# Optimization experiments

Measured on AMD Instinct MI355X. Metric: run time of the kernel, lower is better.

The kernel has to match this reference:

```python
import jax, jax.numpy as jnp
import numpy as np

LOG_STD_MAX = 2.0
LOG_STD_MIN = -5.0
LN_EPS = 1e-5


def layer_norm(x, scale, bias):
    mu = jnp.mean(x, axis=-1, keepdims=True)
    var = jnp.var(x, axis=-1, keepdims=True)
    return (x - mu) * jax.lax.rsqrt(var + LN_EPS) * scale + bias


def setup_inputs() -> dict:
    key = jax.random.key(0)
    B, OBS, ACT, H, M, K = 4096, 256, 32, 512, 16, 4
    ks = jax.random.split(key, 8)
    def w(k, shape, fan_in):
        return (jax.random.normal(k, shape, jnp.float32) / np.sqrt(fan_in)).astype(jnp.float32)
    return {
        "x": jax.random.normal(ks[0], (B, OBS), jnp.float32),
        "gate_W": w(ks[1], (OBS, M), OBS),
        "gate_b": jnp.zeros((M,), jnp.float32),
        "fc1_W": w(ks[2], (OBS, H * M), OBS),
        "fc1_b": jnp.zeros((H * M,), jnp.float32),
        "norm1_scale": jnp.ones((H * M,), jnp.float32),
        "norm1_bias": jnp.zeros((H * M,), jnp.float32),
        "fc2_W": w(ks[3], (H * M, H * M), H * M),
        "fc2_b": jnp.zeros((H * M,), jnp.float32),
        "norm2_scale": jnp.ones((H * M,), jnp.float32),
        "norm2_bias": jnp.zeros((H * M,), jnp.float32),
        "mean_W": w(ks[4], (H, ACT), H),
        "mean_b": jnp.zeros((ACT,), jnp.float32),
        "logstd_W": w(ks[5], (H, ACT), H),
        "logstd_b": jnp.zeros((ACT,), jnp.float32),
        "topk": K,
    }


def reference(x, gate_W, gate_b, fc1_W, fc1_b, norm1_scale, norm1_bias,
              fc2_W, fc2_b, norm2_scale, norm2_bias,
              mean_W, mean_b, logstd_W, logstd_b, topk):
    B = x.shape[0]
    M = gate_W.shape[1]
    # gating: softmax -> topk -> renormalize -> scatter into full [B, M] scores
    gate_scores = jax.nn.softmax(x @ gate_W + gate_b, axis=-1)  # [B, M]
    topk_vals, topk_idx = jax.lax.top_k(gate_scores, topk)       # [B, K]
    topk_vals = topk_vals / jnp.sum(topk_vals, axis=-1, keepdims=True)
    scores = jnp.zeros_like(gate_scores).at[jnp.arange(B)[:, None], topk_idx].set(topk_vals)
    # trunk: Linear -> LayerNorm -> ReLU, twice
    h = jax.nn.relu(layer_norm(x @ fc1_W + fc1_b, norm1_scale, norm1_bias))
    h = jax.nn.relu(layer_norm(h @ fc2_W + fc2_b, norm2_scale, norm2_bias))
    # reshape [B, H*M] -> [B, H, M] (expert m = strided slice), weighted MEAN over experts
    h = h.reshape(B, -1, M)                                      # [B, H, M]
    mixed = jnp.einsum('bhm,bm->bh', h, scores) / M              # mean, not sum
    mean = mixed @ mean_W + mean_b
    log_std = jnp.tanh(mixed @ logstd_W + logstd_b)
    log_std = LOG_STD_MIN + 0.5 * (LOG_STD_MAX - LOG_STD_MIN) * (log_std + 1.0)
    return mean, log_std
```

## Files before the change

kernel.cpp:

```cpp
#include <hip/hip_runtime.h>
#include <hip/hip_bf16.h>

typedef unsigned int u32;
typedef unsigned short u16;
typedef __bf16 bf16x8 __attribute__((ext_vector_type(8)));
typedef float f32x4 __attribute__((ext_vector_type(4)));

__device__ __forceinline__ u16 f2b(float f) {
    __bf16 b = (__bf16)f;
    return __builtin_bit_cast(u16, b);
}
__device__ __forceinline__ float b2f(u16 v) {
    u32 x = ((u32)v) << 16;
    return __builtin_bit_cast(float, x);
}

__device__ __forceinline__ void gld_lds16(const void* g, void* l) {
    __builtin_amdgcn_global_load_lds(
        (const __attribute__((address_space(1))) u32*)(size_t)g,
        (__attribute__((address_space(3))) u32*)(u32)(size_t)l,
        16, 0, 0);
}

#define BARRIER __builtin_amdgcn_s_barrier()
#define LGKM0 asm volatile("s_waitcnt lgkmcnt(0)" ::: "memory")
#define VMC4 asm volatile("s_waitcnt vmcnt(4)" ::: "memory")
#define VMC6 asm volatile("s_waitcnt vmcnt(6)" ::: "memory")
#define VMC0 asm volatile("s_waitcnt vmcnt(0)" ::: "memory")
#define MFMA16(d, a, b) d = __builtin_amdgcn_mfma_f32_16x16x32_bf16(a, b, d, 0, 0, 0)

__global__ __launch_bounds__(256) void castgate_kernel(
    const float* __restrict__ x, const float* __restrict__ gW,
    const float* __restrict__ gb, const int* __restrict__ topk,
    u16* __restrict__ XB, float* __restrict__ scores)
{
    const int t = threadIdx.x;
    {
        int i = blockIdx.x * 256 + t;
        float4 f = reinterpret_cast<const float4*>(x)[i];
        u32 lo = (u32)f2b(f.x) | ((u32)f2b(f.y) << 16);
        u32 hi = (u32)f2b(f.z) | ((u32)f2b(f.w) << 16);
        uint2 o; o.x = lo; o.y = hi;
        reinterpret_cast<uint2*>(XB)[i] = o;
    }
    const int row = blockIdx.x * 4 + (t >> 6);
    const int l = t & 63;
    const int m = l & 15;
    const int q = l >> 4;
    const int Kk = *topk;
    const float* xr = x + (long)row * 256;
    float p = 0.f;
    #pragma unroll
    for (int k4 = 0; k4 < 16; ++k4) {
        f32x4 xv = *reinterpret_cast<const f32x4*>(xr + q * 64 + k4 * 4);
        const int kb = q * 64 + k4 * 4;
        p += xv[0] * gW[(kb + 0) * 16 + m] + xv[1] * gW[(kb + 1) * 16 + m]
           + xv[2] * gW[(kb + 2) * 16 + m] + xv[3] * gW[(kb + 3) * 16 + m];
    }
    p += __shfl_xor(p, 16);
    p += __shfl_xor(p, 32);
    float logit = p + gb[m];
    float mx = logit;
    #pragma unroll
    for (int d = 1; d < 16; d <<= 1) mx = fmaxf(mx, __shfl_xor(mx, d));
    int rank = 0;
    #pragma unroll
    for (int j = 0; j < 16; ++j) {
        float vj = __shfl(logit, (l & 48) | j);
        rank += (vj > logit) || (vj == logit && j < m);
    }
    bool sel = rank < Kk;
    float e = sel ? expf(logit - mx) : 0.f;
    float ssum = e;
    #pragma unroll
    for (int d = 1; d < 16; d <<= 1) ssum += __shfl_xor(ssum, d);
    if (q == 0) scores[row * 16 + m] = e / ssum;
}

__global__ __launch_bounds__(256) void transpose_both_kernel(
    const float* __restrict__ w2, u16* __restrict__ W2T,
    const float* __restrict__ w1, u16* __restrict__ W1T)
{
    __shared__ float tile[64][65];
    const int t = threadIdx.x;
    const int byy = blockIdx.y;
    const float* in;
    u16* outp;
    int R, r0;
    if (byy < 128) { in = w2; outp = W2T; R = 8192; r0 = byy * 64; }
    else           { in = w1; outp = W1T; R = 256;  r0 = (byy - 128) * 64; }
    const int C = 8192;
    const int c0 = blockIdx.x * 64;
    #pragma unroll
    for (int i = 0; i < 4; ++i) {
        int idx = t + i * 256;
        int r = idx >> 4;
        int c = (idx & 15) * 4;
        float4 f = *reinterpret_cast<const float4*>(&in[(long)(r0 + r) * C + c0 + c]);
        tile[r][c] = f.x; tile[r][c + 1] = f.y; tile[r][c + 2] = f.z; tile[r][c + 3] = f.w;
    }
    __syncthreads();
    #pragma unroll
    for (int i = 0; i < 8; ++i) {
        int idx = t + i * 256;
        int rr = idx >> 5;
        int cc = idx & 31;
        u32 p = (u32)f2b(tile[cc * 2 + 0][rr]) | ((u32)f2b(tile[cc * 2 + 1][rr]) << 16);
        *reinterpret_cast<u32*>(&outp[(long)(c0 + rr) * R + r0 + cc * 2]) = p;
    }
}


template<int GRAN>
__device__ __forceinline__ void stage_half(
    const u16* __restrict__ src, int ld, int rowbase, int kk,
    u16* ldsregion, int h, int w, int l)
{
    #pragma unroll
    for (int j = 0; j < 2; ++j) {
        const int c = w * 2 + j;
        const int o = c * 1024 + l * 16;
        const int os = o ^ (((o >> 7) & 7) << 4);
        const int pos = o >> 7;
        const int row = ((pos / GRAN) * 2 + h) * GRAN + (pos & (GRAN - 1));
        const u16* g = src + (long)(rowbase + row) * ld + kk + ((os & 127) >> 1);
        gld_lds16(g, ldsregion + c * 512);
    }
}

__device__ __forceinline__ bf16x8 ldfrag(const u16* region, int pos, int col) {
    const int o = (pos * 128 + col * 2) ^ ((pos & 7) << 4);
    return *reinterpret_cast<const bf16x8*>(reinterpret_cast<const char*>(region) + o);
}

template<int CB>
__device__ __forceinline__ void ktile_group(
    const u16* __restrict__ A, int lda, const u16* __restrict__ BT, int ldb,
    int brow, int bcol, int kkA1, int kkR,
    int wr, int wc, int r4, int q8, int w, int l,
    u16 (&lds)[2][4][8192], f32x4 (&acc)[8][4],
    bf16x8 (&bLu)[2][2], bf16x8 (&bLf)[2][2])
{
    bf16x8 aL[4][2], aH[4][2], bH[2][2];

    #pragma unroll
    for (int m = 0; m < 4; ++m) {
        aL[m][0] = ldfrag(lds[CB][0], wr * 64 + m * 16 + r4, q8);
        aL[m][1] = ldfrag(lds[CB][0], wr * 64 + m * 16 + r4, 32 + q8);
    }
    stage_half<64>(A, lda, brow, kkA1, &lds[1 - CB][1][0], 1, w, l);
    BARRIER; LGKM0;
    __builtin_amdgcn_s_setprio(1);
    #pragma unroll
    for (int m = 0; m < 4; ++m)
        #pragma unroll
        for (int n = 0; n < 2; ++n) {
            MFMA16(acc[m][n], aL[m][0], bLu[n][0]);
            MFMA16(acc[m][n], aL[m][1], bLu[n][1]);
        }
    __builtin_amdgcn_s_setprio(0);
    BARRIER;

    #pragma unroll
    for (int n = 0; n < 2; ++n) {
        bH[n][0] = ldfrag(lds[CB][3], wc * 32 + n * 16 + r4, q8);
        bH[n][1] = ldfrag(lds[CB][3], wc * 32 + n * 16 + r4, 32 + q8);
    }
    stage_half<64>(A, lda, brow, kkR, &lds[CB][0][0], 0, w, l);
    BARRIER; LGKM0;
    __builtin_amdgcn_s_setprio(1);
    #pragma unroll
    for (int m = 0; m < 4; ++m)
        #pragma unroll
        for (int n = 0; n < 2; ++n) {
            MFMA16(acc[m][2 + n], aL[m][0], bH[n][0]);
            MFMA16(acc[m][2 + n], aL[m][1], bH[n][1]);
        }
    __builtin_amdgcn_s_setprio(0);
    BARRIER;

    #pragma unroll
    for (int m = 0; m < 4; ++m) {
        aH[m][0] = ldfrag(lds[CB][1], wr * 64 + m * 16 + r4, q8);
        aH[m][1] = ldfrag(lds[CB][1], wr * 64 + m * 16 + r4, 32 + q8);
    }
    stage_half<32>(BT, ldb, bcol, kkR, &lds[CB][2][0], 0, w, l);
    BARRIER; LGKM0;
    __builtin_amdgcn_s_setprio(1);
    #pragma unroll
    for (int m = 0; m < 4; ++m)
        #pragma unroll
        for (int n = 0; n < 2; ++n) {
            MFMA16(acc[4 + m][2 + n], aH[m][0], bH[n][0]);
            MFMA16(acc[4 + m][2 + n], aH[m][1], bH[n][1]);
        }
    __builtin_amdgcn_s_setprio(0);
    VMC4;
    BARRIER;

    stage_half<32>(BT, ldb, bcol, kkR, &lds[CB][3][0], 1, w, l);
    #pragma unroll
    for (int n = 0; n < 2; ++n) {
        bLf[n][0] = ldfrag(lds[1 - CB][2], wc * 32 + n * 16 + r4, q8);
        bLf[n][1] = ldfrag(lds[1 - CB][2], wc * 32 + n * 16 + r4, 32 + q8);
    }
    __builtin_amdgcn_s_setprio(1);
    #pragma unroll
    for (int m = 0; m < 4; ++m)
        #pragma unroll
        for (int n = 0; n < 2; ++n) {
            MFMA16(acc[4 + m][n], aH[m][0], bLu[n][0]);
            MFMA16(acc[4 + m][n], aH[m][1], bLu[n][1]);
        }
    __builtin_amdgcn_s_setprio(0);
    BARRIER;
}

__global__ __launch_bounds__(512, 2) void gemm256(
    const u16* __restrict__ A, int lda,
    const u16* __restrict__ BT, int ldb,
    u16* __restrict__ C, int ldc, int K)
{
    __shared__ __align__(16) u16 lds[2][4][8192];
    const int t = threadIdx.x;
    const int w = t >> 6, l = t & 63;
    const int wr = w >> 2, wc = w & 3;
    const int r4 = l & 15, q8 = (l >> 4) * 8;
    const int bid = blockIdx.y * 32 + blockIdx.x;
    const int xcd = bid & 7, within = bid >> 3;
    const int by = (xcd >> 2) * 8 + (within >> 3);
    const int bx = (xcd & 3) * 8 + (within & 7);
    const int brow = by * 256, bcol = bx * 256;
    const int NT = K >> 6;

    f32x4 acc[8][4];
    #pragma unroll
    for (int m = 0; m < 8; ++m)
        #pragma unroll
        for (int n = 0; n < 4; ++n)
            acc[m][n] = (f32x4){0.f, 0.f, 0.f, 0.f};

    stage_half<64>(A, lda, brow, 0, &lds[0][0][0], 0, w, l);
    stage_half<32>(BT, ldb, bcol, 0, &lds[0][2][0], 0, w, l);
    stage_half<32>(BT, ldb, bcol, 0, &lds[0][3][0], 1, w, l);
    stage_half<64>(A, lda, brow, 0, &lds[0][1][0], 1, w, l);
    stage_half<64>(A, lda, brow, 64, &lds[1][0][0], 0, w, l);
    stage_half<32>(BT, ldb, bcol, 64, &lds[1][2][0], 0, w, l);
    stage_half<32>(BT, ldb, bcol, 64, &lds[1][3][0], 1, w, l);
    VMC6;
    BARRIER;

    bf16x8 bl0[2][2], bl1[2][2];
    #pragma unroll
    for (int n = 0; n < 2; ++n) {
        bl0[n][0] = ldfrag(lds[0][2], wc * 32 + n * 16 + r4, q8);
        bl0[n][1] = ldfrag(lds[0][2], wc * 32 + n * 16 + r4, 32 + q8);
    }

    for (int i = 0; i < (NT >> 1); ++i) {
        const int U = 2 * i;
        int tV = U + 1;
        int tU2 = U + 2;
        int tV2 = U + 3;
        if (tU2 >= NT) tU2 -= NT;
        if (tV2 >= NT) tV2 -= NT;
        const int kkV = (tV >= NT ? tV - NT : tV) << 6;
        const int kkU2 = tU2 << 6;
        const int kkV2 = tV2 << 6;

        ktile_group<0>(A, lda, BT, ldb, brow, bcol, kkV, kkU2,
                       wr, wc, r4, q8, w, l, lds, acc, bl0, bl1);
        ktile_group<1>(A, lda, BT, ldb, brow, bcol, kkU2, kkV2,
                       wr, wc, r4, q8, w, l, lds, acc, bl1, bl0);
    }

    VMC0;

    const int crow0 = (l >> 4) * 4;
    const int ccol = l & 15;
    #pragma unroll
    for (int m = 0; m < 8; ++m) {
        #pragma unroll
        for (int n = 0; n < 4; ++n) {
            int gr = brow + wr * 128 + m * 16 + crow0;
            int gc = bcol + wc * 64 + n * 16 + ccol;
            #pragma unroll
            for (int r = 0; r < 4; ++r)
                C[(long)(gr + r) * ldc + gc] = f2b(acc[m][n][r]);
        }
    }
}

__global__ __launch_bounds__(256) void ln1_kernel(
    const u16* __restrict__ Y, const float* __restrict__ fcb,
    const float* __restrict__ g, const float* __restrict__ be,
    u16* __restrict__ H)
{
    const int N = 8192;
    const int row = blockIdx.x;
    const int t = threadIdx.x;
    const u16* y = Y + (long)row * N;
    const int base = t * 32;
    float v[32];
    float s = 0.f, s2 = 0.f;
    #pragma unroll
    for (int j = 0; j < 4; ++j) {
        uint4 q = *reinterpret_cast<const uint4*>(y + base + j * 8);
        f32x4 cA = *reinterpret_cast<const f32x4*>(fcb + base + j * 8);
        f32x4 cB = *reinterpret_cast<const f32x4*>(fcb + base + j * 8 + 4);
        const u32 ww[4] = {q.x, q.y, q.z, q.w};
        const float cb[8] = {cA[0], cA[1], cA[2], cA[3], cB[0], cB[1], cB[2], cB[3]};
        #pragma unroll
        for (int e = 0; e < 4; ++e) {
            float a0 = b2f((u16)(ww[e] & 0xffff)) + cb[e * 2];
            float a1 = b2f((u16)(ww[e] >> 16)) + cb[e * 2 + 1];
            v[j * 8 + e * 2] = a0; v[j * 8 + e * 2 + 1] = a1;
            s += a0 + a1;
            s2 += a0 * a0 + a1 * a1;
        }
    }
    #pragma unroll
    for (int d = 32; d > 0; d >>= 1) { s += __shfl_down(s, d); s2 += __shfl_down(s2, d); }
    __shared__ float red[8];
    if ((t & 63) == 0) { red[t >> 6] = s; red[4 + (t >> 6)] = s2; }
    __syncthreads();
    s = red[0] + red[1] + red[2] + red[3];
    s2 = red[4] + red[5] + red[6] + red[7];
    float mu = s * (1.f / N);
    float var = s2 * (1.f / N) - mu * mu;
    float rs = rsqrtf(var + 1e-5f);
    __align__(16) u16 o[32];
    #pragma unroll
    for (int j = 0; j < 4; ++j) {
        f32x4 gA = *reinterpret_cast<const f32x4*>(g + base + j * 8);
        f32x4 gB = *reinterpret_cast<const f32x4*>(g + base + j * 8 + 4);
        f32x4 eA = *reinterpret_cast<const f32x4*>(be + base + j * 8);
        f32x4 eB = *reinterpret_cast<const f32x4*>(be + base + j * 8 + 4);
        const float gg[8] = {gA[0], gA[1], gA[2], gA[3], gB[0], gB[1], gB[2], gB[3]};
        const float ee[8] = {eA[0], eA[1], eA[2], eA[3], eB[0], eB[1], eB[2], eB[3]};
        #pragma unroll
        for (int k = 0; k < 8; ++k) {
            float z = (v[j * 8 + k] - mu) * rs * gg[k] + ee[k];
            o[j * 8 + k] = f2b(fmaxf(z, 0.f));
        }
    }
    u16* h = H + (long)row * N + base;
    #pragma unroll
    for (int j = 0; j < 4; ++j)
        *reinterpret_cast<uint4*>(h + j * 8) = *reinterpret_cast<const uint4*>(&o[j * 8]);
}

__global__ __launch_bounds__(256) void ln2_mix_heads_kernel(
    const u16* __restrict__ Y, const float* __restrict__ fcb,
    const float* __restrict__ g, const float* __restrict__ be,
    const float* __restrict__ scores,
    const float* __restrict__ mW, const float* __restrict__ mb,
    const float* __restrict__ sW, const float* __restrict__ sb,
    float* __restrict__ out)
{
    const int N = 8192;
    const int B = 4096;
    const int row = blockIdx.x;
    const int t = threadIdx.x;
    const u16* y = Y + (long)row * N;
    const int base = t * 32;
    __shared__ float sc[16];
    if (t < 16) sc[t] = scores[row * 16 + t];
    float v[32];
    float s = 0.f, s2 = 0.f;
    #pragma unroll
    for (int j = 0; j < 4; ++j) {
        uint4 q = *reinterpret_cast<const uint4*>(y + base + j * 8);
        f32x4 cA = *reinterpret_cast<const f32x4*>(fcb + base + j * 8);
        f32x4 cB = *reinterpret_cast<const f32x4*>(fcb + base + j * 8 + 4);
        const u32 ww[4] = {q.x, q.y, q.z, q.w};
        const float cb[8] = {cA[0], cA[1], cA[2], cA[3], cB[0], cB[1], cB[2], cB[3]};
        #pragma unroll
        for (int e = 0; e < 4; ++e) {
            float a0 = b2f((u16)(ww[e] & 0xffff)) + cb[e * 2];
            float a1 = b2f((u16)(ww[e] >> 16)) + cb[e * 2 + 1];
            v[j * 8 + e * 2] = a0; v[j * 8 + e * 2 + 1] = a1;
            s += a0 + a1;
            s2 += a0 * a0 + a1 * a1;
        }
    }
    #pragma unroll
    for (int d = 32; d > 0; d >>= 1) { s += __shfl_down(s, d); s2 += __shfl_down(s2, d); }
    __shared__ float red[8];
    if ((t & 63) == 0) { red[t >> 6] = s; red[4 + (t >> 6)] = s2; }
    __syncthreads();
    s = red[0] + red[1] + red[2] + red[3];
    s2 = red[4] + red[5] + red[6] + red[7];
    float mu = s * (1.f / N);
    float var = s2 * (1.f / N) - mu * mu;
    float rs = rsqrtf(var + 1e-5f);
    float m0 = 0.f, m1 = 0.f;
    #pragma unroll
    for (int j = 0; j < 4; ++j) {
        f32x4 g0 = *reinterpret_cast<const f32x4*>(g + base + j * 4);
        f32x4 e0 = *reinterpret_cast<const f32x4*>(be + base + j * 4);
        f32x4 g1 = *reinterpret_cast<const f32x4*>(g + base + 16 + j * 4);
        f32x4 e1 = *reinterpret_cast<const f32x4*>(be + base + 16 + j * 4);
        #pragma unroll
        for (int k = 0; k < 4; ++k) {
            int m = j * 4 + k;
            float z0 = fmaxf((v[m] - mu) * rs * g0[k] + e0[k], 0.f);
            float z1 = fmaxf((v[16 + m] - mu) * rs * g1[k] + e1[k], 0.f);
            m0 += z0 * sc[m];
            m1 += z1 * sc[m];
        }
    }
    __shared__ float mix[512];
    mix[2 * t]     = m0 * (1.f / 16.f);
    mix[2 * t + 1] = m1 * (1.f / 16.f);
    __syncthreads();
    const int a = t & 31;
    const int seg = t >> 5;
    float pm = 0.f, ps = 0.f;
    #pragma unroll 4
    for (int h = seg * 64; h < seg * 64 + 64; ++h) {
        float xv = mix[h];
        pm += xv * mW[h * 32 + a];
        ps += xv * sW[h * 32 + a];
    }
    __shared__ float prm[8][32];
    __shared__ float prs[8][32];
    prm[seg][a] = pm;
    prs[seg][a] = ps;
    __syncthreads();
    if (t < 32) {
        float am = mb[t];
        #pragma unroll
        for (int ss = 0; ss < 8; ++ss) am += prm[ss][t];
        out[(long)row * 32 + t] = am;
    } else if (t < 64) {
        int aa = t - 32;
        float as = sb[aa];
        #pragma unroll
        for (int ss = 0; ss < 8; ++ss) as += prs[ss][aa];
        float ts = tanhf(as);
        out[(long)B * 32 + (long)row * 32 + aa] = -5.0f + 3.5f * (ts + 1.0f);
    }
}

extern "C" void kernel_launch(void* const* d_in, const int* in_sizes, int n_in,
                              void* d_out, int out_size, void* d_ws, size_t ws_size,
                              hipStream_t stream) {
    const float* x   = (const float*)d_in[0];
    const float* gW  = (const float*)d_in[1];
    const float* gb  = (const float*)d_in[2];
    const float* w1  = (const float*)d_in[3];
    const float* b1  = (const float*)d_in[4];
    const float* g1  = (const float*)d_in[5];
    const float* be1 = (const float*)d_in[6];
    const float* w2  = (const float*)d_in[7];
    const float* b2  = (const float*)d_in[8];
    const float* g2  = (const float*)d_in[9];
    const float* be2 = (const float*)d_in[10];
    const float* mW  = (const float*)d_in[11];
    const float* mb  = (const float*)d_in[12];
    const float* sW  = (const float*)d_in[13];
    const float* sb  = (const float*)d_in[14];
    const int* topk  = (const int*)d_in[15];
    float* out = (float*)d_out;

    char* ws = (char*)d_ws;
    u16* W2T = (u16*)ws;            ws += (long)8192 * 8192 * 2;
    u16* Yb = (u16*)ws;             ws += (long)4096 * 8192 * 2;
    u16* H1 = (u16*)ws;             ws += (long)4096 * 8192 * 2;
    u16* W1T = (u16*)ws;            ws += (long)8192 * 256 * 2;
    u16* XB = (u16*)ws;             ws += (long)4096 * 256 * 2;
    float* SCR = (float*)ws;        ws += (long)4096 * 16 * 4;

    castgate_kernel<<<1024, 256, 0, stream>>>(x, gW, gb, topk, XB, SCR);
    transpose_both_kernel<<<dim3(128, 132), 256, 0, stream>>>(w2, W2T, w1, W1T);

    gemm256<<<dim3(32, 16), 512, 0, stream>>>(XB, 256, W1T, 256, Yb, 8192, 256);
    ln1_kernel<<<4096, 256, 0, stream>>>(Yb, b1, g1, be1, H1);

    gemm256<<<dim3(32, 16), 512, 0, stream>>>(H1, 8192, W2T, 8192, Yb, 8192, 8192);
    ln2_mix_heads_kernel<<<4096, 256, 0, stream>>>(Yb, b2, g2, be2, SCR,
                                                   mW, mb, sW, sb, out);
}
```

Before: 706.0 us.

## Use 16 waves per GEMM block with smaller per-wave tiles; widen transpose stores

The 256x256 GEMM tile now runs on 1024 threads (16 waves in a 4x4 grid) instead of 512, so each wave owns a 64x64 sub-tile with 16 accumulators instead of 32. Each wave issues one global-to-LDS load per stage instead of two, and the vmcnt waits are lowered to match. The aim is more waves to hide latency and lower register pressure per wave, at the cost of more LDS fragment reads per MFMA and more barrier participants. The transpose kernel also switches to 8-byte stores.

```diff
diff --git a/kernel.cpp b/kernel.cpp
--- a/kernel.cpp
+++ b/kernel.cpp
@@ -24,8 +24,8 @@
 
 #define BARRIER __builtin_amdgcn_s_barrier()
 #define LGKM0 asm volatile("s_waitcnt lgkmcnt(0)" ::: "memory")
-#define VMC4 asm volatile("s_waitcnt vmcnt(4)" ::: "memory")
-#define VMC6 asm volatile("s_waitcnt vmcnt(6)" ::: "memory")
+#define VMC2 asm volatile("s_waitcnt vmcnt(2)" ::: "memory")
+#define VMC3 asm volatile("s_waitcnt vmcnt(3)" ::: "memory")
 #define VMC0 asm volatile("s_waitcnt vmcnt(0)" ::: "memory")
 #define MFMA16(d, a, b) d = __builtin_amdgcn_mfma_f32_16x16x32_bf16(a, b, d, 0, 0, 0)
 
@@ -101,31 +101,28 @@
     }
     __syncthreads();
     #pragma unroll
-    for (int i = 0; i < 8; ++i) {
+    for (int i = 0; i < 4; ++i) {
         int idx = t + i * 256;
-        int rr = idx >> 5;
-        int cc = idx & 31;
-        u32 p = (u32)f2b(tile[cc * 2 + 0][rr]) | ((u32)f2b(tile[cc * 2 + 1][rr]) << 16);
-        *reinterpret_cast<u32*>(&outp[(long)(c0 + rr) * R + r0 + cc * 2]) = p;
-    }
-}
-
-
-template<int GRAN>
-__device__ __forceinline__ void stage_half(
+        int rr = idx >> 4;
+        int cc = idx & 15;
+        u32 p0 = (u32)f2b(tile[cc * 4 + 0][rr]) | ((u32)f2b(tile[cc * 4 + 1][rr]) << 16);
+        u32 p1 = (u32)f2b(tile[cc * 4 + 2][rr]) | ((u32)f2b(tile[cc * 4 + 3][rr]) << 16);
+        uint2 o2; o2.x = p0; o2.y = p1;
+        *reinterpret_cast<uint2*>(&outp[(long)(c0 + rr) * R + r0 + cc * 4]) = o2;
+    }
+}
+
+
+__device__ __forceinline__ void stage16(
     const u16* __restrict__ src, int ld, int rowbase, int kk,
     u16* ldsregion, int h, int w, int l)
 {
-    #pragma unroll
-    for (int j = 0; j < 2; ++j) {
-        const int c = w * 2 + j;
-        const int o = c * 1024 + l * 16;
-        const int os = o ^ (((o >> 7) & 7) << 4);
-        const int pos = o >> 7;
-        const int row = ((pos / GRAN) * 2 + h) * GRAN + (pos & (GRAN - 1));
-        const u16* g = src + (long)(rowbase + row) * ld + kk + ((os & 127) >> 1);
-        gld_lds16(g, ldsregion + c * 512);
-    }
+    const int o = w * 1024 + l * 16;
+    const int os = o ^ (((o >> 7) & 7) << 4);
+    const int pos = o >> 7;
+    const int row = ((pos >> 4) * 2 + h) * 16 + (pos & 15);
+    const u16* g = src + (long)(rowbase + row) * ld + kk + ((os & 127) >> 1);
+    gld_lds16(g, ldsregion + w * 512);
 }
 
 __device__ __forceinline__ bf16x8 ldfrag(const u16* region, int pos, int col) {
@@ -138,85 +135,85 @@
     const u16* __restrict__ A, int lda, const u16* __restrict__ BT, int ldb,
     int brow, int bcol, int kkA1, int kkR,
     int wr, int wc, int r4, int q8, int w, int l,
-    u16 (&lds)[2][4][8192], f32x4 (&acc)[8][4],
-    bf16x8 (&bLu)[2][2], bf16x8 (&bLf)[2][2])
-{
-    bf16x8 aL[4][2], aH[4][2], bH[2][2];
-
-    #pragma unroll
-    for (int m = 0; m < 4; ++m) {
-        aL[m][0] = ldfrag(lds[CB][0], wr * 64 + m * 16 + r4, q8);
-        aL[m][1] = ldfrag(lds[CB][0], wr * 64 + m * 16 + r4, 32 + q8);
-    }
-    stage_half<64>(A, lda, brow, kkA1, &lds[1 - CB][1][0], 1, w, l);
+    u16 (&lds)[2][4][8192], f32x4 (&acc)[4][4],
+    bf16x8 (&bEu)[2][2], bf16x8 (&bEf)[2][2])
+{
+    bf16x8 aE[2][2], aO[2][2], bO[2][2];
+
+    #pragma unroll
+    for (int mi = 0; mi < 2; ++mi) {
+        aE[mi][0] = ldfrag(lds[CB][0], (wr * 2 + mi) * 16 + r4, q8);
+        aE[mi][1] = ldfrag(lds[CB][0], (wr * 2 + mi) * 16 + r4, 32 + q8);
+    }
+    stage16(A, lda, brow, kkA1, &lds[1 - CB][1][0], 1, w, l);
     BARRIER; LGKM0;
     __builtin_amdgcn_s_setprio(1);
     #pragma unroll
-    for (int m = 0; m < 4; ++m)
-        #pragma unroll
-        for (int n = 0; n < 2; ++n) {
-            MFMA16(acc[m][n], aL[m][0], bLu[n][0]);
-            MFMA16(acc[m][n], aL[m][1], bLu[n][1]);
+    for (int mi = 0; mi < 2; ++mi)
+        #pragma unroll
+        for (int ni = 0; ni < 2; ++ni) {
+            MFMA16(acc[2 * mi][2 * ni], aE[mi][0], bEu[ni][0]);
+            MFMA16(acc[2 * mi][2 * ni], aE[mi][1], bEu[ni][1]);
         }
     __builtin_amdgcn_s_setprio(0);
     BARRIER;
 
     #pragma unroll
-    for (int n = 0; n < 2; ++n) {
-        bH[n][0] = ldfrag(lds[CB][3], wc * 32 + n * 16 + r4, q8);
-        bH[n][1] = ldfrag(lds[CB][3], wc * 32 + n * 16 + r4, 32 + q8);
-    }
-    stage_half<64>(A, lda, brow, kkR, &lds[CB][0][0], 0, w, l);
+    for (int ni = 0; ni < 2; ++ni) {
+        bO[ni][0] = ldfrag(lds[CB][3], (wc * 2 + ni) * 16 + r4, q8);
+        bO[ni][1] = ldfrag(lds[CB][3], (wc * 2 + ni) * 16 + r4, 32 + q8);
+    }
+    stage16(A, lda, brow, kkR, &lds[CB][0][0], 0, w, l);
     BARRIER; LGKM0;
     __builtin_amdgcn_s_setprio(1);
     #pragma unroll
-    for (int m = 0; m < 4; ++m)
-        #pragma unroll
-        for (int n = 0; n < 2; ++n) {
-            MFMA16(acc[m][2 + n], aL[m][0], bH[n][0]);
-            MFMA16(acc[m][2 + n], aL[m][1], bH[n][1]);
+    for (int mi = 0; mi < 2; ++mi)
+        #pragma unroll
+        for (int ni = 0; ni < 2; ++ni) {
+            MFMA16(acc[2 * mi][2 * ni + 1], aE[mi][0], bO[ni][0]);
+            MFMA16(acc[2 * mi][2 * ni + 1], aE[mi][1], bO[ni][1]);
         }
     __builtin_amdgcn_s_setprio(0);
     BARRIER;
 
     #pragma unroll
-    for (int m = 0; m < 4; ++m) {
-        aH[m][0] = ldfrag(lds[CB][1], wr * 64 + m * 16 + r4, q8);
-        aH[m][1] = ldfrag(lds[CB][1], wr * 64 + m * 16 + r4, 32 + q8);
-    }
-    stage_half<32>(BT, ldb, bcol, kkR, &lds[CB][2][0], 0, w, l);
+    for (int mi = 0; mi < 2; ++mi) {
+        aO[mi][0] = ldfrag(lds[CB][1], (wr * 2 + mi) * 16 + r4, q8);
+        aO[mi][1] = ldfrag(lds[CB][1], (wr * 2 + mi) * 16 + r4, 32 + q8);
+    }
+    stage16(BT, ldb, bcol, kkR, &lds[CB][2][0], 0, w, l);
     BARRIER; LGKM0;
     __builtin_amdgcn_s_setprio(1);
     #pragma unroll
-    for (int m = 0; m < 4; ++m)
-        #pragma unroll
-        for (int n = 0; n < 2; ++n) {
-            MFMA16(acc[4 + m][2 + n], aH[m][0], bH[n][0]);
-            MFMA16(acc[4 + m][2 + n], aH[m][1], bH[n][1]);
+    for (int mi = 0; mi < 2; ++mi)
+        #pragma unroll
+        for (int ni = 0; ni < 2; ++ni) {
+            MFMA16(acc[2 * mi + 1][2 * ni + 1], aO[mi][0], bO[ni][0]);
+            MFMA16(acc[2 * mi + 1][2 * ni + 1], aO[mi][1], bO[ni][1]);
         }
     __builtin_amdgcn_s_setprio(0);
-    VMC4;
+    VMC2;
     BARRIER;
 
-    stage_half<32>(BT, ldb, bcol, kkR, &lds[CB][3][0], 1, w, l);
-    #pragma unroll
-    for (int n = 0; n < 2; ++n) {
-        bLf[n][0] = ldfrag(lds[1 - CB][2], wc * 32 + n * 16 + r4, q8);
-        bLf[n][1] = ldfrag(lds[1 - CB][2], wc * 32 + n * 16 + r4, 32 + q8);
+    stage16(BT, ldb, bcol, kkR, &lds[CB][3][0], 1, w, l);
+    #pragma unroll
+    for (int ni = 0; ni < 2; ++ni) {
+        bEf[ni][0] = ldfrag(lds[1 - CB][2], (wc * 2 + ni) * 16 + r4, q8);
+        bEf[ni][1] = ldfrag(lds[1 - CB][2], (wc * 2 + ni) * 16 + r4, 32 + q8);
     }
     __builtin_amdgcn_s_setprio(1);
     #pragma unroll
-    for (int m = 0; m < 4; ++m)
-        #pragma unroll
-        for (int n = 0; n < 2; ++n) {
-            MFMA16(acc[4 + m][n], aH[m][0], bLu[n][0]);
-            MFMA16(acc[4 + m][n], aH[m][1], bLu[n][1]);
+    for (int mi = 0; mi < 2; ++mi)
+        #pragma unroll
+        for (int ni = 0; ni < 2; ++ni) {
+            MFMA16(acc[2 * mi + 1][2 * ni], aO[mi][0], bEu[ni][0]);
+            MFMA16(acc[2 * mi + 1][2 * ni], aO[mi][1], bEu[ni][1]);
         }
     __builtin_amdgcn_s_setprio(0);
     BARRIER;
 }
 
-__global__ __launch_bounds__(512, 2) void gemm256(
+__global__ __launch_bounds__(1024, 4) void gemm256(
     const u16* __restrict__ A, int lda,
     const u16* __restrict__ BT, int ldb,
     u16* __restrict__ C, int ldc, int K)
@@ -233,28 +230,28 @@
     const int brow = by * 256, bcol = bx * 256;
     const int NT = K >> 6;
 
-    f32x4 acc[8][4];
-    #pragma unroll
-    for (int m = 0; m < 8; ++m)
+    f32x4 acc[4][4];
+    #pragma unroll
+    for (int m = 0; m < 4; ++m)
         #pragma unroll
         for (int n = 0; n < 4; ++n)
             acc[m][n] = (f32x4){0.f, 0.f, 0.f, 0.f};
 
-    stage_half<64>(A, lda, brow, 0, &lds[0][0][0], 0, w, l);
-    stage_half<32>(BT, ldb, bcol, 0, &lds[0][2][0], 0, w, l);
-    stage_half<32>(BT, ldb, bcol, 0, &lds[0][3][0], 1, w, l);
-    stage_half<64>(A, lda, brow, 0, &lds[0][1][0], 1, w, l);
-    stage_half<64>(A, lda, brow, 64, &lds[1][0][0], 0, w, l);
-    stage_half<32>(BT, ldb, bcol, 64, &lds[1][2][0], 0, w, l);
-    stage_half<32>(BT, ldb, bcol, 64, &lds[1][3][0], 1, w, l);
-    VMC6;
+    stage16(A, lda, brow, 0, &lds[0][0][0], 0, w, l);
+    stage16(BT, ldb, bcol, 0, &lds[0][2][0], 0, w, l);
+    stage16(BT, ldb, bcol, 0, &lds[0][3][0], 1, w, l);
+    stage16(A, lda, brow, 0, &lds[0][1][0], 1, w, l);
+    stage16(A, lda, brow, 64, &lds[1][0][0], 0, w, l);
+    stage16(BT, ldb, bcol, 64, &lds[1][2][0], 0, w, l);
+    stage16(BT, ldb, bcol, 64, &lds[1][3][0], 1, w, l);
+    VMC3;
     BARRIER;
 
     bf16x8 bl0[2][2], bl1[2][2];
     #pragma unroll
-    for (int n = 0; n < 2; ++n) {
-        bl0[n][0] = ldfrag(lds[0][2], wc * 32 + n * 16 + r4, q8);
-        bl0[n][1] = ldfrag(lds[0][2], wc * 32 + n * 16 + r4, 32 + q8);
+    for (int ni = 0; ni < 2; ++ni) {
+        bl0[ni][0] = ldfrag(lds[0][2], (wc * 2 + ni) * 16 + r4, q8);
+        bl0[ni][1] = ldfrag(lds[0][2], (wc * 2 + ni) * 16 + r4, 32 + q8);
     }
 
     for (int i = 0; i < (NT >> 1); ++i) {
@@ -279,10 +276,10 @@
     const int crow0 = (l >> 4) * 4;
     const int ccol = l & 15;
     #pragma unroll
-    for (int m = 0; m < 8; ++m) {
+    for (int m = 0; m < 4; ++m) {
         #pragma unroll
         for (int n = 0; n < 4; ++n) {
-            int gr = brow + wr * 128 + m * 16 + crow0;
+            int gr = brow + wr * 64 + m * 16 + crow0;
             int gc = bcol + wc * 64 + n * 16 + ccol;
             #pragma unroll
             for (int r = 0; r < 4; ++r)
@@ -475,10 +472,10 @@
     castgate_kernel<<<1024, 256, 0, stream>>>(x, gW, gb, topk, XB, SCR);
     transpose_both_kernel<<<dim3(128, 132), 256, 0, stream>>>(w2, W2T, w1, W1T);
 
-    gemm256<<<dim3(32, 16), 512, 0, stream>>>(XB, 256, W1T, 256, Yb, 8192, 256);
+    gemm256<<<dim3(32, 16), 1024, 0, stream>>>(XB, 256, W1T, 256, Yb, 8192, 256);
     ln1_kernel<<<4096, 256, 0, stream>>>(Yb, b1, g1, be1, H1);
 
-    gemm256<<<dim3(32, 16), 512, 0, stream>>>(H1, 8192, W2T, 8192, Yb, 8192, 8192);
+    gemm256<<<dim3(32, 16), 1024, 0, stream>>>(H1, 8192, W2T, 8192, Yb, 8192, 8192);
     ln2_mix_heads_kernel<<<4096, 256, 0, stream>>>(Yb, b2, g2, be2, SCR,
                                                    mW, mb, sW, sb, out);
 }
```

Measured after the change: 1.619 ms. +129.3%, slower.
